# Kernel optimization log

Measured on AMD Instinct MI355X. Metric: run time of the kernel, lower is better.

## Reference

```python
import jax, jax.numpy as jnp
import numpy as np

N = 50000
E = 800000
D_IN = 128
D_HID = 256


def setup_inputs() -> dict:
    key = jax.random.key(0)
    ks = jax.random.split(key, 12)
    s = 0.02
    return {
        "node_features": jax.random.normal(ks[0], (N, D_IN), dtype=jnp.float32),
        "edge_index": jax.random.randint(ks[1], (2, E), 0, N, dtype=jnp.int64),
        # layer 0 (input_dim -> hidden)
        "eps0": jnp.zeros((), dtype=jnp.float32),
        "W1_0": jax.random.normal(ks[2], (D_IN, D_HID), dtype=jnp.float32) * s,
        "b1_0": jnp.zeros((D_HID,), dtype=jnp.float32),
        "W2_0": jax.random.normal(ks[3], (D_HID, D_HID), dtype=jnp.float32) * s,
        "b2_0": jnp.zeros((D_HID,), dtype=jnp.float32),
        # layer 1 (hidden -> hidden)
        "eps1": jnp.zeros((), dtype=jnp.float32),
        "W1_1": jax.random.normal(ks[4], (D_HID, D_HID), dtype=jnp.float32) * s,
        "b1_1": jnp.zeros((D_HID,), dtype=jnp.float32),
        "W2_1": jax.random.normal(ks[5], (D_HID, D_HID), dtype=jnp.float32) * s,
        "b2_1": jnp.zeros((D_HID,), dtype=jnp.float32),
        # fc_out (hidden -> input_dim)
        "Wo": jax.random.normal(ks[6], (D_HID, D_IN), dtype=jnp.float32) * s,
        "bo": jnp.zeros((D_IN,), dtype=jnp.float32),
    }


def _gin_layer(x, src, dst, eps, W1, b1, W2, b2):
    # gather neighbor features + scatter-add into destination nodes
    agg = jnp.zeros_like(x).at[dst].add(x[src])  # [N, d]
    h = (1.0 + eps) * x + agg
    h = jax.nn.relu(h @ W1 + b1)
    return h @ W2 + b2


def reference(node_features, edge_index, eps0, W1_0, b1_0, W2_0, b2_0,
              eps1, W1_1, b1_1, W2_1, b2_1, Wo, bo):
    src, dst = edge_index[0], edge_index[1]
    h = _gin_layer(node_features, src, dst, eps0, W1_0, b1_0, W2_0, b2_0)
    h = _gin_layer(h, src, dst, eps1, W1_1, b1_1, W2_1, b2_1)
    return h @ Wo + bo  # [N, input_dim]
```

## Files before the change

### kernel.cpp

```cpp
#include <hip/hip_runtime.h>

#define NN 50000
#define NE 800000
#define DIN 128
#define DHID 256
#define MAXDEG 128

typedef __bf16 bf16x8 __attribute__((ext_vector_type(8)));
typedef float f32x4 __attribute__((ext_vector_type(4)));

static __device__ __forceinline__ unsigned short f2bf(float f) {
    unsigned u = __float_as_uint(f);
    unsigned r = 0x7fffu + ((u >> 16) & 1u);
    return (unsigned short)((u + r) >> 16);
}
static __device__ __forceinline__ float blo(unsigned u) { return __uint_as_float(u << 16); }
static __device__ __forceinline__ float bhi(unsigned u) { return __uint_as_float(u & 0xffff0000u); }


__global__ void bucket_kernel(const int* __restrict__ src, const int* __restrict__ dst,
                              int* __restrict__ cnt, int* __restrict__ srcs, int E) {
    int i8 = (blockIdx.x * blockDim.x + threadIdx.x) * 8;
    if (i8 >= E) return;
    int4 da = *(const int4*)&dst[i8];
    int4 db = *(const int4*)&dst[i8 + 4];
    int4 sa = *(const int4*)&src[i8];
    int4 sb = *(const int4*)&src[i8 + 4];
    int t0 = atomicAdd(&cnt[da.x], 1);
    int t1 = atomicAdd(&cnt[da.y], 1);
    int t2 = atomicAdd(&cnt[da.z], 1);
    int t3 = atomicAdd(&cnt[da.w], 1);
    int t4 = atomicAdd(&cnt[db.x], 1);
    int t5 = atomicAdd(&cnt[db.y], 1);
    int t6 = atomicAdd(&cnt[db.z], 1);
    int t7 = atomicAdd(&cnt[db.w], 1);
    if (t0 < MAXDEG) srcs[(size_t)da.x * MAXDEG + t0] = sa.x;
    if (t1 < MAXDEG) srcs[(size_t)da.y * MAXDEG + t1] = sa.y;
    if (t2 < MAXDEG) srcs[(size_t)da.z * MAXDEG + t2] = sa.z;
    if (t3 < MAXDEG) srcs[(size_t)da.w * MAXDEG + t3] = sa.w;
    if (t4 < MAXDEG) srcs[(size_t)db.x * MAXDEG + t4] = sb.x;
    if (t5 < MAXDEG) srcs[(size_t)db.y * MAXDEG + t5] = sb.y;
    if (t6 < MAXDEG) srcs[(size_t)db.z * MAXDEG + t6] = sb.z;
    if (t7 < MAXDEG) srcs[(size_t)db.w * MAXDEG + t7] = sb.w;
}


__global__ void prep_kernel(const float* __restrict__ x, unsigned short* __restrict__ xb,
                            int* __restrict__ cnt,
                            const float* __restrict__ W1_0, const float* __restrict__ W2_0,
                            const float* __restrict__ W1_1, const float* __restrict__ W2_1,
                            const float* __restrict__ Wo,
                            unsigned short* __restrict__ w10t, unsigned short* __restrict__ w20t,
                            unsigned short* __restrict__ w11t, unsigned short* __restrict__ w21t,
                            unsigned short* __restrict__ wot) {
    int i = blockIdx.x * blockDim.x + threadIdx.x;
    if (i < NN) cnt[i] = 0;
    if (i < 262144) {
        const float* W; unsigned short* Wt; int K, N, idx;
        if (i < 32768)        { W = W1_0; Wt = w10t; K = 128; N = 256; idx = i; }
        else if (i < 98304)   { W = W2_0; Wt = w20t; K = 256; N = 256; idx = i - 32768; }
        else if (i < 163840)  { W = W1_1; Wt = w11t; K = 256; N = 256; idx = i - 98304; }
        else if (i < 229376)  { W = W2_1; Wt = w21t; K = 256; N = 256; idx = i - 163840; }
        else                  { W = Wo;   Wt = wot;  K = 256; N = 128; idx = i - 229376; }
        int k = idx / N;
        int n = idx - k * N;
        Wt[(size_t)n * K + k] = f2bf(W[idx]);
    }
    if (i * 4 < NN * DIN) {
        float4 v = *(const float4*)(x + (size_t)i * 4);
        ushort4 o;
        o.x = f2bf(v.x); o.y = f2bf(v.y); o.z = f2bf(v.z); o.w = f2bf(v.w);
        *(ushort4*)(xb + (size_t)i * 4) = o;
    }
}


template <int D>
__global__ void agg_bf16_kernel(const unsigned short* __restrict__ x, const int* __restrict__ cnt,
                                const int* __restrict__ srcs, const float* __restrict__ eps_p,
                                unsigned short* __restrict__ out, int n) {
    constexpr int G = (D == 128) ? 4 : 2;
    constexpr int L = 64 / G;
    constexpr int RQ = D / 8;
    int tid = blockIdx.x * blockDim.x + threadIdx.x;
    int wid = tid >> 6;
    int lane = threadIdx.x & 63;
    int group = lane / L;
    int li = lane % L;
    int node = wid * G + group;
    if (node >= n) return;
    int deg = cnt[node]; if (deg > MAXDEG) deg = MAXDEG;
    const int* sp = srcs + (size_t)node * MAXDEG;
    const uint4* xp = (const uint4*)x;
    float e = 1.0f + eps_p[0];

    float a[8], b[8];
    #pragma unroll
    for (int j = 0; j < 8; j++) { a[j] = 0.f; b[j] = 0.f; }

    int i = 0;
    for (; i + 8 <= deg; i += 8) {
        int4 s0 = *(const int4*)&sp[i];
        int4 s1 = *(const int4*)&sp[i + 4];
        uint4 v0 = xp[(size_t)s0.x * RQ + li];
        uint4 v1 = xp[(size_t)s0.y * RQ + li];
        uint4 v2 = xp[(size_t)s0.z * RQ + li];
        uint4 v3 = xp[(size_t)s0.w * RQ + li];
        uint4 v4 = xp[(size_t)s1.x * RQ + li];
        uint4 v5 = xp[(size_t)s1.y * RQ + li];
        uint4 v6 = xp[(size_t)s1.z * RQ + li];
        uint4 v7 = xp[(size_t)s1.w * RQ + li];
        a[0] += blo(v0.x); a[1] += bhi(v0.x); a[2] += blo(v0.y); a[3] += bhi(v0.y);
        a[4] += blo(v0.z); a[5] += bhi(v0.z); a[6] += blo(v0.w); a[7] += bhi(v0.w);
        b[0] += blo(v1.x); b[1] += bhi(v1.x); b[2] += blo(v1.y); b[3] += bhi(v1.y);
        b[4] += blo(v1.z); b[5] += bhi(v1.z); b[6] += blo(v1.w); b[7] += bhi(v1.w);
        a[0] += blo(v2.x); a[1] += bhi(v2.x); a[2] += blo(v2.y); a[3] += bhi(v2.y);
        a[4] += blo(v2.z); a[5] += bhi(v2.z); a[6] += blo(v2.w); a[7] += bhi(v2.w);
        b[0] += blo(v3.x); b[1] += bhi(v3.x); b[2] += blo(v3.y); b[3] += bhi(v3.y);
        b[4] += blo(v3.z); b[5] += bhi(v3.z); b[6] += blo(v3.w); b[7] += bhi(v3.w);
        a[0] += blo(v4.x); a[1] += bhi(v4.x); a[2] += blo(v4.y); a[3] += bhi(v4.y);
        a[4] += blo(v4.z); a[5] += bhi(v4.z); a[6] += blo(v4.w); a[7] += bhi(v4.w);
        b[0] += blo(v5.x); b[1] += bhi(v5.x); b[2] += blo(v5.y); b[3] += bhi(v5.y);
        b[4] += blo(v5.z); b[5] += bhi(v5.z); b[6] += blo(v5.w); b[7] += bhi(v5.w);
        a[0] += blo(v6.x); a[1] += bhi(v6.x); a[2] += blo(v6.y); a[3] += bhi(v6.y);
        a[4] += blo(v6.z); a[5] += bhi(v6.z); a[6] += blo(v6.w); a[7] += bhi(v6.w);
        b[0] += blo(v7.x); b[1] += bhi(v7.x); b[2] += blo(v7.y); b[3] += bhi(v7.y);
        b[4] += blo(v7.z); b[5] += bhi(v7.z); b[6] += blo(v7.w); b[7] += bhi(v7.w);
    }
    for (; i + 4 <= deg; i += 4) {
        int4 s = *(const int4*)&sp[i];
        uint4 v0 = xp[(size_t)s.x * RQ + li];
        uint4 v1 = xp[(size_t)s.y * RQ + li];
        uint4 v2 = xp[(size_t)s.z * RQ + li];
        uint4 v3 = xp[(size_t)s.w * RQ + li];
        a[0] += blo(v0.x); a[1] += bhi(v0.x); a[2] += blo(v0.y); a[3] += bhi(v0.y);
        a[4] += blo(v0.z); a[5] += bhi(v0.z); a[6] += blo(v0.w); a[7] += bhi(v0.w);
        b[0] += blo(v1.x); b[1] += bhi(v1.x); b[2] += blo(v1.y); b[3] += bhi(v1.y);
        b[4] += blo(v1.z); b[5] += bhi(v1.z); b[6] += blo(v1.w); b[7] += bhi(v1.w);
        a[0] += blo(v2.x); a[1] += bhi(v2.x); a[2] += blo(v2.y); a[3] += bhi(v2.y);
        a[4] += blo(v2.z); a[5] += bhi(v2.z); a[6] += blo(v2.w); a[7] += bhi(v2.w);
        b[0] += blo(v3.x); b[1] += bhi(v3.x); b[2] += blo(v3.y); b[3] += bhi(v3.y);
        b[4] += blo(v3.z); b[5] += bhi(v3.z); b[6] += blo(v3.w); b[7] += bhi(v3.w);
    }
    for (; i < deg; i++) {
        uint4 v = xp[(size_t)sp[i] * RQ + li];
        a[0] += blo(v.x); a[1] += bhi(v.x); a[2] += blo(v.y); a[3] += bhi(v.y);
        a[4] += blo(v.z); a[5] += bhi(v.z); a[6] += blo(v.w); a[7] += bhi(v.w);
    }
    uint4 xv = xp[(size_t)node * RQ + li];
    a[0] += b[0] + e * blo(xv.x); a[1] += b[1] + e * bhi(xv.x);
    a[2] += b[2] + e * blo(xv.y); a[3] += b[3] + e * bhi(xv.y);
    a[4] += b[4] + e * blo(xv.z); a[5] += b[5] + e * bhi(xv.z);
    a[6] += b[6] + e * blo(xv.w); a[7] += b[7] + e * bhi(xv.w);
    uint4 o;
    o.x = (unsigned)f2bf(a[0]) | ((unsigned)f2bf(a[1]) << 16);
    o.y = (unsigned)f2bf(a[2]) | ((unsigned)f2bf(a[3]) << 16);
    o.z = (unsigned)f2bf(a[4]) | ((unsigned)f2bf(a[5]) << 16);
    o.w = (unsigned)f2bf(a[6]) | ((unsigned)f2bf(a[7]) << 16);
    ((uint4*)out)[(size_t)node * RQ + li] = o;
}


template <int K1, int THREE>
__global__ __launch_bounds__(256) void mlp_fused(
        const unsigned short* __restrict__ A,
        const unsigned short* __restrict__ W1t, const float* __restrict__ b1,
        const unsigned short* __restrict__ W2t, const float* __restrict__ b2,
        const unsigned short* __restrict__ W3t, const float* __restrict__ b3,
        unsigned short* __restrict__ Cb, float* __restrict__ Cf, int M) {
    constexpr int NKS1 = K1 / 32;
    __shared__ __align__(16) unsigned short H[64 * 256];

    const int lane = threadIdx.x & 63;
    const int w = threadIdx.x >> 6;
    const int quad = lane >> 4;
    const int l16 = lane & 15;
    const size_t rowbase = (size_t)blockIdx.x * 64;

    f32x4 acc[4][4];

    #pragma unroll
    for (int j = 0; j < 4; j++)
        #pragma unroll
        for (int nt = 0; nt < 4; nt++) acc[j][nt] = (f32x4)(0.f);
    #pragma unroll 2
    for (int ks = 0; ks < NKS1; ks++) {
        bf16x8 bw[4];
        #pragma unroll
        for (int nt = 0; nt < 4; nt++)
            bw[nt] = *(const bf16x8*)&W1t[(size_t)(w * 64 + nt * 16 + l16) * K1 + ks * 32 + quad * 8];
        #pragma unroll
        for (int j = 0; j < 4; j++) {
            bf16x8 af = *(const bf16x8*)&A[(rowbase + j * 16 + l16) * K1 + ks * 32 + quad * 8];
            #pragma unroll
            for (int nt = 0; nt < 4; nt++)
                acc[j][nt] = __builtin_amdgcn_mfma_f32_16x16x32_bf16(bw[nt], af, acc[j][nt], 0, 0, 0);
        }
    }
    {
        f32x4 bvv[4];
        #pragma unroll
        for (int nt = 0; nt < 4; nt++)
            bvv[nt] = *(const f32x4*)&b1[w * 64 + nt * 16 + quad * 4];
        #pragma unroll
        for (int j = 0; j < 4; j++) {
            int r = j * 16 + l16;
            #pragma unroll
            for (int nt = 0; nt < 4; nt++) {
                f32x4 v = acc[j][nt] + bvv[nt];
                v[0] = fmaxf(v[0], 0.f); v[1] = fmaxf(v[1], 0.f);
                v[2] = fmaxf(v[2], 0.f); v[3] = fmaxf(v[3], 0.f);
                int c = w * 8 + nt * 2 + (quad >> 1);
                int cs = c ^ (r & 7);
                uint2 o;
                o.x = (unsigned)f2bf(v[0]) | ((unsigned)f2bf(v[1]) << 16);
                o.y = (unsigned)f2bf(v[2]) | ((unsigned)f2bf(v[3]) << 16);
                *(uint2*)&H[r * 256 + cs * 8 + (quad & 1) * 4] = o;
            }
        }
    }
    __syncthreads();

    #pragma unroll
    for (int j = 0; j < 4; j++)
        #pragma unroll
        for (int nt = 0; nt < 4; nt++) acc[j][nt] = (f32x4)(0.f);
    #pragma unroll 2
    for (int ks = 0; ks < 8; ks++) {
        bf16x8 bw[4];
        #pragma unroll
        for (int nt = 0; nt < 4; nt++)
            bw[nt] = *(const bf16x8*)&W2t[(size_t)(w * 64 + nt * 16 + l16) * 256 + ks * 32 + quad * 8];
        #pragma unroll
        for (int j = 0; j < 4; j++) {
            int r = j * 16 + l16;
            int cs = (ks * 4 + quad) ^ (r & 7);
            bf16x8 af = *(const bf16x8*)&H[r * 256 + cs * 8];
            #pragma unroll
            for (int nt = 0; nt < 4; nt++)
                acc[j][nt] = __builtin_amdgcn_mfma_f32_16x16x32_bf16(bw[nt], af, acc[j][nt], 0, 0, 0);
        }
    }
    {
        f32x4 bvv[4];
        #pragma unroll
        for (int nt = 0; nt < 4; nt++)
            bvv[nt] = *(const f32x4*)&b2[w * 64 + nt * 16 + quad * 4];
        if constexpr (!THREE) {
            #pragma unroll
            for (int j = 0; j < 4; j++) {
                size_t gm = rowbase + j * 16 + l16;
                if (gm < (size_t)M) {
                    #pragma unroll
                    for (int nt = 0; nt < 4; nt++) {
                        f32x4 v = acc[j][nt] + bvv[nt];
                        uint2 o;
                        o.x = (unsigned)f2bf(v[0]) | ((unsigned)f2bf(v[1]) << 16);
                        o.y = (unsigned)f2bf(v[2]) | ((unsigned)f2bf(v[3]) << 16);
                        *(uint2*)&Cb[gm * 256 + w * 64 + nt * 16 + quad * 4] = o;
                    }
                }
            }
        } else {
            __syncthreads();
            #pragma unroll
            for (int j = 0; j < 4; j++) {
                int r = j * 16 + l16;
                #pragma unroll
                for (int nt = 0; nt < 4; nt++) {
                    f32x4 v = acc[j][nt] + bvv[nt];
                    int c = w * 8 + nt * 2 + (quad >> 1);
                    int cs = c ^ (r & 7);
                    uint2 o;
                    o.x = (unsigned)f2bf(v[0]) | ((unsigned)f2bf(v[1]) << 16);
                    o.y = (unsigned)f2bf(v[2]) | ((unsigned)f2bf(v[3]) << 16);
                    *(uint2*)&H[r * 256 + cs * 8 + (quad & 1) * 4] = o;
                }
            }
            __syncthreads();
        }
    }

    if constexpr (THREE) {
        f32x4 acc3[4][2];
        #pragma unroll
        for (int j = 0; j < 4; j++)
            #pragma unroll
            for (int nt = 0; nt < 2; nt++) acc3[j][nt] = (f32x4)(0.f);
        #pragma unroll 2
        for (int ks = 0; ks < 8; ks++) {
            bf16x8 bw[2];
            #pragma unroll
            for (int nt = 0; nt < 2; nt++)
                bw[nt] = *(const bf16x8*)&W3t[(size_t)(w * 32 + nt * 16 + l16) * 256 + ks * 32 + quad * 8];
            #pragma unroll
            for (int j = 0; j < 4; j++) {
                int r = j * 16 + l16;
                int cs = (ks * 4 + quad) ^ (r & 7);
                bf16x8 af = *(const bf16x8*)&H[r * 256 + cs * 8];
                #pragma unroll
                for (int nt = 0; nt < 2; nt++)
                    acc3[j][nt] = __builtin_amdgcn_mfma_f32_16x16x32_bf16(bw[nt], af, acc3[j][nt], 0, 0, 0);
            }
        }
        f32x4 bv3[2];
        #pragma unroll
        for (int nt = 0; nt < 2; nt++)
            bv3[nt] = *(const f32x4*)&b3[w * 32 + nt * 16 + quad * 4];
        #pragma unroll
        for (int j = 0; j < 4; j++) {
            size_t gm = rowbase + j * 16 + l16;
            if (gm < (size_t)M) {
                #pragma unroll
                for (int nt = 0; nt < 2; nt++) {
                    f32x4 v = acc3[j][nt] + bv3[nt];
                    *(f32x4*)&Cf[gm * 128 + w * 32 + nt * 16 + quad * 4] = v;
                }
            }
        }
    }
}


static inline size_t align256(size_t v) { return (v + 255) & ~(size_t)255; }

extern "C" void kernel_launch(void* const* d_in, const int* in_sizes, int n_in,
                              void* d_out, int out_size, void* d_ws, size_t ws_size,
                              hipStream_t stream) {
    const float* x        = (const float*)d_in[0];
    const int*   ei       = (const int*)d_in[1];
    const float* eps0     = (const float*)d_in[2];
    const float* W1_0     = (const float*)d_in[3];
    const float* b1_0     = (const float*)d_in[4];
    const float* W2_0     = (const float*)d_in[5];
    const float* b2_0     = (const float*)d_in[6];
    const float* eps1     = (const float*)d_in[7];
    const float* W1_1     = (const float*)d_in[8];
    const float* b1_1     = (const float*)d_in[9];
    const float* W2_1     = (const float*)d_in[10];
    const float* b2_1     = (const float*)d_in[11];
    const float* Wo       = (const float*)d_in[12];
    const float* bo       = (const float*)d_in[13];
    float* out            = (float*)d_out;

    const int* srcE = ei;
    const int* dstE = ei + NE;

    char* p = (char*)d_ws;
    size_t o = 0;
    int* cnt  = (int*)(p + o); o = align256(o + (size_t)NN * 4);
    int* srcs = (int*)(p + o); o = align256(o + (size_t)NN * MAXDEG * 4);
    unsigned short* xb   = (unsigned short*)(p + o); o = align256(o + (size_t)NN * DIN * 2);
    unsigned short* w10t = (unsigned short*)(p + o); o = align256(o + (size_t)DHID * DIN * 2);
    unsigned short* w20t = (unsigned short*)(p + o); o = align256(o + (size_t)DHID * DHID * 2);
    unsigned short* w11t = (unsigned short*)(p + o); o = align256(o + (size_t)DHID * DHID * 2);
    unsigned short* w21t = (unsigned short*)(p + o); o = align256(o + (size_t)DHID * DHID * 2);
    unsigned short* wot  = (unsigned short*)(p + o); o = align256(o + (size_t)DIN * DHID * 2);
    unsigned short* bufA = (unsigned short*)(p + o); o = align256(o + (size_t)NN * DHID * 2 + 65536);
    unsigned short* bufB = (unsigned short*)(p + o); o = align256(o + (size_t)NN * DHID * 2 + 65536);

    prep_kernel<<<(NN * DIN / 4 + 255) / 256, 256, 0, stream>>>(
        x, xb, cnt, W1_0, W2_0, W1_1, W2_1, Wo, w10t, w20t, w11t, w21t, wot);
    bucket_kernel<<<(NE / 8 + 255) / 256, 256, 0, stream>>>(srcE, dstE, cnt, srcs, NE);

    int aggBlocks128 = ((NN + 3) / 4 + 3) / 4;
    int aggBlocks256 = ((NN + 1) / 2 + 3) / 4;
    int mlpBlocks = (NN + 63) / 64;

    agg_bf16_kernel<DIN><<<aggBlocks128, 256, 0, stream>>>(xb, cnt, srcs, eps0, bufA, NN);
    mlp_fused<128, 0><<<mlpBlocks, 256, 0, stream>>>(
        bufA, w10t, b1_0, w20t, b2_0, nullptr, nullptr, bufB, nullptr, NN);

    agg_bf16_kernel<DHID><<<aggBlocks256, 256, 0, stream>>>(bufB, cnt, srcs, eps1, bufA, NN);
    mlp_fused<256, 1><<<mlpBlocks, 256, 0, stream>>>(
        bufA, w11t, b1_1, w21t, b2_1, wot, bo, nullptr, out, NN);
}
```

Before: 332.0 us.

## Fuse neighbor aggregation into MLP kernel via swizzled shared-memory tile

```diff
diff --git a/kernel.cpp b/kernel.cpp
--- a/kernel.cpp
+++ b/kernel.cpp
@@ -75,100 +75,19 @@
 }
 
 
-template <int D>
-__global__ void agg_bf16_kernel(const unsigned short* __restrict__ x, const int* __restrict__ cnt,
-                                const int* __restrict__ srcs, const float* __restrict__ eps_p,
-                                unsigned short* __restrict__ out, int n) {
-    constexpr int G = (D == 128) ? 4 : 2;
-    constexpr int L = 64 / G;
-    constexpr int RQ = D / 8;
-    int tid = blockIdx.x * blockDim.x + threadIdx.x;
-    int wid = tid >> 6;
-    int lane = threadIdx.x & 63;
-    int group = lane / L;
-    int li = lane % L;
-    int node = wid * G + group;
-    if (node >= n) return;
-    int deg = cnt[node]; if (deg > MAXDEG) deg = MAXDEG;
-    const int* sp = srcs + (size_t)node * MAXDEG;
-    const uint4* xp = (const uint4*)x;
-    float e = 1.0f + eps_p[0];
-
-    float a[8], b[8];
-    #pragma unroll
-    for (int j = 0; j < 8; j++) { a[j] = 0.f; b[j] = 0.f; }
-
-    int i = 0;
-    for (; i + 8 <= deg; i += 8) {
-        int4 s0 = *(const int4*)&sp[i];
-        int4 s1 = *(const int4*)&sp[i + 4];
-        uint4 v0 = xp[(size_t)s0.x * RQ + li];
-        uint4 v1 = xp[(size_t)s0.y * RQ + li];
-        uint4 v2 = xp[(size_t)s0.z * RQ + li];
-        uint4 v3 = xp[(size_t)s0.w * RQ + li];
-        uint4 v4 = xp[(size_t)s1.x * RQ + li];
-        uint4 v5 = xp[(size_t)s1.y * RQ + li];
-        uint4 v6 = xp[(size_t)s1.z * RQ + li];
-        uint4 v7 = xp[(size_t)s1.w * RQ + li];
-        a[0] += blo(v0.x); a[1] += bhi(v0.x); a[2] += blo(v0.y); a[3] += bhi(v0.y);
-        a[4] += blo(v0.z); a[5] += bhi(v0.z); a[6] += blo(v0.w); a[7] += bhi(v0.w);
-        b[0] += blo(v1.x); b[1] += bhi(v1.x); b[2] += blo(v1.y); b[3] += bhi(v1.y);
-        b[4] += blo(v1.z); b[5] += bhi(v1.z); b[6] += blo(v1.w); b[7] += bhi(v1.w);
-        a[0] += blo(v2.x); a[1] += bhi(v2.x); a[2] += blo(v2.y); a[3] += bhi(v2.y);
-        a[4] += blo(v2.z); a[5] += bhi(v2.z); a[6] += blo(v2.w); a[7] += bhi(v2.w);
-        b[0] += blo(v3.x); b[1] += bhi(v3.x); b[2] += blo(v3.y); b[3] += bhi(v3.y);
-        b[4] += blo(v3.z); b[5] += bhi(v3.z); b[6] += blo(v3.w); b[7] += bhi(v3.w);
-        a[0] += blo(v4.x); a[1] += bhi(v4.x); a[2] += blo(v4.y); a[3] += bhi(v4.y);
-        a[4] += blo(v4.z); a[5] += bhi(v4.z); a[6] += blo(v4.w); a[7] += bhi(v4.w);
-        b[0] += blo(v5.x); b[1] += bhi(v5.x); b[2] += blo(v5.y); b[3] += bhi(v5.y);
-        b[4] += blo(v5.z); b[5] += bhi(v5.z); b[6] += blo(v5.w); b[7] += bhi(v5.w);
-        a[0] += blo(v6.x); a[1] += bhi(v6.x); a[2] += blo(v6.y); a[3] += bhi(v6.y);
-        a[4] += blo(v6.z); a[5] += bhi(v6.z); a[6] += blo(v6.w); a[7] += bhi(v6.w);
-        b[0] += blo(v7.x); b[1] += bhi(v7.x); b[2] += blo(v7.y); b[3] += bhi(v7.y);
-        b[4] += blo(v7.z); b[5] += bhi(v7.z); b[6] += blo(v7.w); b[7] += bhi(v7.w);
-    }
-    for (; i + 4 <= deg; i += 4) {
-        int4 s = *(const int4*)&sp[i];
-        uint4 v0 = xp[(size_t)s.x * RQ + li];
-        uint4 v1 = xp[(size_t)s.y * RQ + li];
-        uint4 v2 = xp[(size_t)s.z * RQ + li];
-        uint4 v3 = xp[(size_t)s.w * RQ + li];
-        a[0] += blo(v0.x); a[1] += bhi(v0.x); a[2] += blo(v0.y); a[3] += bhi(v0.y);
-        a[4] += blo(v0.z); a[5] += bhi(v0.z); a[6] += blo(v0.w); a[7] += bhi(v0.w);
-        b[0] += blo(v1.x); b[1] += bhi(v1.x); b[2] += blo(v1.y); b[3] += bhi(v1.y);
-        b[4] += blo(v1.z); b[5] += bhi(v1.z); b[6] += blo(v1.w); b[7] += bhi(v1.w);
-        a[0] += blo(v2.x); a[1] += bhi(v2.x); a[2] += blo(v2.y); a[3] += bhi(v2.y);
-        a[4] += blo(v2.z); a[5] += bhi(v2.z); a[6] += blo(v2.w); a[7] += bhi(v2.w);
-        b[0] += blo(v3.x); b[1] += bhi(v3.x); b[2] += blo(v3.y); b[3] += bhi(v3.y);
-        b[4] += blo(v3.z); b[5] += bhi(v3.z); b[6] += blo(v3.w); b[7] += bhi(v3.w);
-    }
-    for (; i < deg; i++) {
-        uint4 v = xp[(size_t)sp[i] * RQ + li];
-        a[0] += blo(v.x); a[1] += bhi(v.x); a[2] += blo(v.y); a[3] += bhi(v.y);
-        a[4] += blo(v.z); a[5] += bhi(v.z); a[6] += blo(v.w); a[7] += bhi(v.w);
-    }
-    uint4 xv = xp[(size_t)node * RQ + li];
-    a[0] += b[0] + e * blo(xv.x); a[1] += b[1] + e * bhi(xv.x);
-    a[2] += b[2] + e * blo(xv.y); a[3] += b[3] + e * bhi(xv.y);
-    a[4] += b[4] + e * blo(xv.z); a[5] += b[5] + e * bhi(xv.z);
-    a[6] += b[6] + e * blo(xv.w); a[7] += b[7] + e * bhi(xv.w);
-    uint4 o;
-    o.x = (unsigned)f2bf(a[0]) | ((unsigned)f2bf(a[1]) << 16);
-    o.y = (unsigned)f2bf(a[2]) | ((unsigned)f2bf(a[3]) << 16);
-    o.z = (unsigned)f2bf(a[4]) | ((unsigned)f2bf(a[5]) << 16);
-    o.w = (unsigned)f2bf(a[6]) | ((unsigned)f2bf(a[7]) << 16);
-    ((uint4*)out)[(size_t)node * RQ + li] = o;
-}
-
-
 template <int K1, int THREE>
 __global__ __launch_bounds__(256) void mlp_fused(
-        const unsigned short* __restrict__ A,
+        const unsigned short* __restrict__ X,
+        const int* __restrict__ cnt, const int* __restrict__ srcs,
+        const float* __restrict__ eps_p,
         const unsigned short* __restrict__ W1t, const float* __restrict__ b1,
         const unsigned short* __restrict__ W2t, const float* __restrict__ b2,
         const unsigned short* __restrict__ W3t, const float* __restrict__ b3,
         unsigned short* __restrict__ Cb, float* __restrict__ Cf, int M) {
     constexpr int NKS1 = K1 / 32;
+    constexpr int G = (K1 == 128) ? 4 : 2;
+    constexpr int L = 64 / G;
+    constexpr int RQ = K1 / 8;
     __shared__ __align__(16) unsigned short H[64 * 256];
 
     const int lane = threadIdx.x & 63;
@@ -177,6 +96,86 @@
     const int l16 = lane & 15;
     const size_t rowbase = (size_t)blockIdx.x * 64;
 
+    {
+        const int group = lane / L;
+        const int li = lane % L;
+        const uint4* xp = (const uint4*)X;
+        const float e = 1.0f + eps_p[0];
+        for (int p = 0; p < 16 / G; p++) {
+            const int r = w * 16 + p * G + group;
+            const size_t node = rowbase + r;
+            if (node < (size_t)M) {
+                int deg = cnt[node]; if (deg > MAXDEG) deg = MAXDEG;
+                const int* sp = srcs + (size_t)node * MAXDEG;
+                float a[8], b[8];
+                #pragma unroll
+                for (int j = 0; j < 8; j++) { a[j] = 0.f; b[j] = 0.f; }
+                int i = 0;
+                for (; i + 8 <= deg; i += 8) {
+                    int4 s0 = *(const int4*)&sp[i];
+                    int4 s1 = *(const int4*)&sp[i + 4];
+                    uint4 v0 = xp[(size_t)s0.x * RQ + li];
+                    uint4 v1 = xp[(size_t)s0.y * RQ + li];
+                    uint4 v2 = xp[(size_t)s0.z * RQ + li];
+                    uint4 v3 = xp[(size_t)s0.w * RQ + li];
+                    uint4 v4 = xp[(size_t)s1.x * RQ + li];
+                    uint4 v5 = xp[(size_t)s1.y * RQ + li];
+                    uint4 v6 = xp[(size_t)s1.z * RQ + li];
+                    uint4 v7 = xp[(size_t)s1.w * RQ + li];
+                    a[0] += blo(v0.x); a[1] += bhi(v0.x); a[2] += blo(v0.y); a[3] += bhi(v0.y);
+                    a[4] += blo(v0.z); a[5] += bhi(v0.z); a[6] += blo(v0.w); a[7] += bhi(v0.w);
+                    b[0] += blo(v1.x); b[1] += bhi(v1.x); b[2] += blo(v1.y); b[3] += bhi(v1.y);
+                    b[4] += blo(v1.z); b[5] += bhi(v1.z); b[6] += blo(v1.w); b[7] += bhi(v1.w);
+                    a[0] += blo(v2.x); a[1] += bhi(v2.x); a[2] += blo(v2.y); a[3] += bhi(v2.y);
+                    a[4] += blo(v2.z); a[5] += bhi(v2.z); a[6] += blo(v2.w); a[7] += bhi(v2.w);
+                    b[0] += blo(v3.x); b[1] += bhi(v3.x); b[2] += blo(v3.y); b[3] += bhi(v3.y);
+                    b[4] += blo(v3.z); b[5] += bhi(v3.z); b[6] += blo(v3.w); b[7] += bhi(v3.w);
+                    a[0] += blo(v4.x); a[1] += bhi(v4.x); a[2] += blo(v4.y); a[3] += bhi(v4.y);
+                    a[4] += blo(v4.z); a[5] += bhi(v4.z); a[6] += blo(v4.w); a[7] += bhi(v4.w);
+                    b[0] += blo(v5.x); b[1] += bhi(v5.x); b[2] += blo(v5.y); b[3] += bhi(v5.y);
+                    b[4] += blo(v5.z); b[5] += bhi(v5.z); b[6] += blo(v5.w); b[7] += bhi(v5.w);
+                    a[0] += blo(v6.x); a[1] += bhi(v6.x); a[2] += blo(v6.y); a[3] += bhi(v6.y);
+                    a[4] += blo(v6.z); a[5] += bhi(v6.z); a[6] += blo(v6.w); a[7] += bhi(v6.w);
+                    b[0] += blo(v7.x); b[1] += bhi(v7.x); b[2] += blo(v7.y); b[3] += bhi(v7.y);
+                    b[4] += blo(v7.z); b[5] += bhi(v7.z); b[6] += blo(v7.w); b[7] += bhi(v7.w);
+                }
+                for (; i + 4 <= deg; i += 4) {
+                    int4 s = *(const int4*)&sp[i];
+                    uint4 v0 = xp[(size_t)s.x * RQ + li];
+                    uint4 v1 = xp[(size_t)s.y * RQ + li];
+                    uint4 v2 = xp[(size_t)s.z * RQ + li];
+                    uint4 v3 = xp[(size_t)s.w * RQ + li];
+                    a[0] += blo(v0.x); a[1] += bhi(v0.x); a[2] += blo(v0.y); a[3] += bhi(v0.y);
+                    a[4] += blo(v0.z); a[5] += bhi(v0.z); a[6] += blo(v0.w); a[7] += bhi(v0.w);
+                    b[0] += blo(v1.x); b[1] += bhi(v1.x); b[2] += blo(v1.y); b[3] += bhi(v1.y);
+                    b[4] += blo(v1.z); b[5] += bhi(v1.z); b[6] += blo(v1.w); b[7] += bhi(v1.w);
+                    a[0] += blo(v2.x); a[1] += bhi(v2.x); a[2] += blo(v2.y); a[3] += bhi(v2.y);
+                    a[4] += blo(v2.z); a[5] += bhi(v2.z); a[6] += blo(v2.w); a[7] += bhi(v2.w);
+                    b[0] += blo(v3.x); b[1] += bhi(v3.x); b[2] += blo(v3.y); b[3] += bhi(v3.y);
+                    b[4] += blo(v3.z); b[5] += bhi(v3.z); b[6] += blo(v3.w); b[7] += bhi(v3.w);
+                }
+                for (; i < deg; i++) {
+                    uint4 v = xp[(size_t)sp[i] * RQ + li];
+                    a[0] += blo(v.x); a[1] += bhi(v.x); a[2] += blo(v.y); a[3] += bhi(v.y);
+                    a[4] += blo(v.z); a[5] += bhi(v.z); a[6] += blo(v.w); a[7] += bhi(v.w);
+                }
+                uint4 xv = xp[(size_t)node * RQ + li];
+                a[0] += b[0] + e * blo(xv.x); a[1] += b[1] + e * bhi(xv.x);
+                a[2] += b[2] + e * blo(xv.y); a[3] += b[3] + e * bhi(xv.y);
+                a[4] += b[4] + e * blo(xv.z); a[5] += b[5] + e * bhi(xv.z);
+                a[6] += b[6] + e * blo(xv.w); a[7] += b[7] + e * bhi(xv.w);
+                uint4 o;
+                o.x = (unsigned)f2bf(a[0]) | ((unsigned)f2bf(a[1]) << 16);
+                o.y = (unsigned)f2bf(a[2]) | ((unsigned)f2bf(a[3]) << 16);
+                o.z = (unsigned)f2bf(a[4]) | ((unsigned)f2bf(a[5]) << 16);
+                o.w = (unsigned)f2bf(a[6]) | ((unsigned)f2bf(a[7]) << 16);
+                const int cs = li ^ (r & 7);
+                *(uint4*)&H[r * K1 + cs * 8] = o;
+            }
+        }
+    }
+    __syncthreads();
+
     f32x4 acc[4][4];
 
     #pragma unroll
@@ -191,12 +190,15 @@
             bw[nt] = *(const bf16x8*)&W1t[(size_t)(w * 64 + nt * 16 + l16) * K1 + ks * 32 + quad * 8];
         #pragma unroll
         for (int j = 0; j < 4; j++) {
-            bf16x8 af = *(const bf16x8*)&A[(rowbase + j * 16 + l16) * K1 + ks * 32 + quad * 8];
+            int r = j * 16 + l16;
+            int cs = (ks * 4 + quad) ^ (r & 7);
+            bf16x8 af = *(const bf16x8*)&H[r * K1 + cs * 8];
             #pragma unroll
             for (int nt = 0; nt < 4; nt++)
                 acc[j][nt] = __builtin_amdgcn_mfma_f32_16x16x32_bf16(bw[nt], af, acc[j][nt], 0, 0, 0);
         }
     }
+    __syncthreads();
     {
         f32x4 bvv[4];
         #pragma unroll
@@ -356,22 +358,17 @@
     unsigned short* w11t = (unsigned short*)(p + o); o = align256(o + (size_t)DHID * DHID * 2);
     unsigned short* w21t = (unsigned short*)(p + o); o = align256(o + (size_t)DHID * DHID * 2);
     unsigned short* wot  = (unsigned short*)(p + o); o = align256(o + (size_t)DIN * DHID * 2);
-    unsigned short* bufA = (unsigned short*)(p + o); o = align256(o + (size_t)NN * DHID * 2 + 65536);
-    unsigned short* bufB = (unsigned short*)(p + o); o = align256(o + (size_t)NN * DHID * 2 + 65536);
+    unsigned short* bufB = (unsigned short*)(p + o); o = align256(o + (size_t)NN * DHID * 2);
 
     prep_kernel<<<(NN * DIN / 4 + 255) / 256, 256, 0, stream>>>(
         x, xb, cnt, W1_0, W2_0, W1_1, W2_1, Wo, w10t, w20t, w11t, w21t, wot);
     bucket_kernel<<<(NE / 8 + 255) / 256, 256, 0, stream>>>(srcE, dstE, cnt, srcs, NE);
 
-    int aggBlocks128 = ((NN + 3) / 4 + 3) / 4;
-    int aggBlocks256 = ((NN + 1) / 2 + 3) / 4;
     int mlpBlocks = (NN + 63) / 64;
 
-    agg_bf16_kernel<DIN><<<aggBlocks128, 256, 0, stream>>>(xb, cnt, srcs, eps0, bufA, NN);
     mlp_fused<128, 0><<<mlpBlocks, 256, 0, stream>>>(
-        bufA, w10t, b1_0, w20t, b2_0, nullptr, nullptr, bufB, nullptr, NN);
-
-    agg_bf16_kernel<DHID><<<aggBlocks256, 256, 0, stream>>>(bufB, cnt, srcs, eps1, bufA, NN);
+        xb, cnt, srcs, eps0, w10t, b1_0, w20t, b2_0, nullptr, nullptr, bufB, nullptr, NN);
+
     mlp_fused<256, 1><<<mlpBlocks, 256, 0, stream>>>(
-        bufA, w11t, b1_1, w21t, b2_1, wot, bo, nullptr, out, NN);
-}
+        bufB, cnt, srcs, eps1, w11t, b1_1, w21t, b2_1, wot, bo, nullptr, out, NN);
+}
```

Result: no change. 336.2 us (+1.3%).
